# Kernel tuning notes

Hardware: AMD Instinct MI355X
Metric: run time of the kernel (lower is better)

## Reference

```python
import jax, jax.numpy as jnp
import numpy as np

HEADS = 16

def setup_inputs() -> dict:
    key = jax.random.key(0)
    k1, k2, k3 = jax.random.split(key, 3)
    B, T, C = 4, 2048, 1024
    s = 0.02
    return {
        "x": jax.random.normal(k1, (B, T, C), dtype=jnp.float32),
        "W_qkv": jax.random.normal(k2, (C, 3 * C), dtype=jnp.float32) * s,
        "b_qkv": jnp.zeros((3 * C,), dtype=jnp.float32),
        "W_pr": jax.random.normal(k3, (C, C), dtype=jnp.float32) * s,
        "b_pr": jnp.zeros((C,), dtype=jnp.float32),
    }

def reference(x, W_qkv, b_qkv, W_pr, b_pr):
    B, T, C = x.shape
    H = HEADS
    hd = C // H
    qkv = x @ W_qkv + b_qkv                     # [B,T,3C]
    q, k, v = jnp.split(qkv, 3, axis=-1)
    # [B,T,C] -> [B,H,T,hd]
    q = q.reshape(B, T, H, hd).transpose(0, 2, 1, 3)
    k = k.reshape(B, T, H, hd).transpose(0, 2, 1, 3)
    v = v.reshape(B, T, H, hd).transpose(0, 2, 1, 3)
    att = jnp.einsum('bhqd,bhkd->bhqk', q, k) * (1.0 / jnp.sqrt(jnp.float32(hd)))
    causal = jnp.tril(jnp.ones((T, T), dtype=bool))
    att = jnp.where(causal[None, None, :, :], att, jnp.float32(-jnp.inf))
    att = jax.nn.softmax(att, axis=-1)
    y = jnp.einsum('bhqk,bhkd->bhqd', att, v)   # [B,H,T,hd]
    y = y.transpose(0, 2, 1, 3).reshape(B, T, C)  # merge heads
    return y @ W_pr + b_pr
```

## Files before the change

kernel.cpp:

```cpp
#include <hip/hip_runtime.h>


typedef __attribute__((ext_vector_type(8))) short bf16x8;
typedef __attribute__((ext_vector_type(4))) float f32x4;

#define MFMA16(a, b, c) __builtin_amdgcn_mfma_f32_16x16x32_bf16(a, b, c, 0, 0, 0)

#define QK_SCALE 0.1803368801111244f

__device__ __forceinline__ unsigned short f2bf(float f) {
    union { float f; unsigned u; } v; v.f = f;
    unsigned r = v.u + 0x7fffu + ((v.u >> 16) & 1u);
    return (unsigned short)(r >> 16);
}

typedef __attribute__((address_space(1))) const unsigned int guint;
typedef __attribute__((address_space(3))) unsigned int luint;
__device__ __forceinline__ void gload16(const void* g, void* l) {
    __builtin_amdgcn_global_load_lds((guint*)g, (luint*)l, 16, 0, 0);
}

__device__ __forceinline__ float exp2_hw(float x) {
    float y;
    asm("v_exp_f32 %0, %1" : "=v"(y) : "v"(x));
    return y;
}

__device__ __forceinline__ unsigned cvt_pk_bf16(float lo, float hi) {
    unsigned w;
    asm("v_cvt_pk_bf16_f32 %0, %1, %2" : "=v"(w) : "v"(lo), "v"(hi));
    return w;
}

__global__ __launch_bounds__(256) void k_prep(
    const float* __restrict__ x, unsigned short* __restrict__ xb,
    const float* __restrict__ Wqkv, unsigned short* __restrict__ Wqt,
    const float* __restrict__ Wpr, unsigned short* __restrict__ Wpt) {
    __shared__ unsigned short tile[32][33];
    const int b = blockIdx.x;
    if (b < 8192) {
        int i = b * 256 + threadIdx.x;
        float4 v = reinterpret_cast<const float4*>(x)[i];
        ushort4 o;
        o.x = f2bf(v.x); o.y = f2bf(v.y); o.z = f2bf(v.z); o.w = f2bf(v.w);
        reinterpret_cast<ushort4*>(xb)[i] = o;
        return;
    }
    const float* W; unsigned short* Wt; int K, N, idx;
    if (b < 11264) { W = Wqkv; Wt = Wqt; K = 1024; N = 3072; idx = b - 8192;  }
    else           { W = Wpr;  Wt = Wpt; K = 1024; N = 1024; idx = b - 11264; }
    const int nb = N / 32;
    const int bn = (idx % nb) * 32, bk = (idx / nb) * 32;
    int tx = threadIdx.x & 31, ty = threadIdx.x >> 5;
#pragma unroll
    for (int i = 0; i < 32; i += 8)
        tile[ty + i][tx] = f2bf(W[(size_t)(bk + ty + i) * N + bn + tx]);
    __syncthreads();
#pragma unroll
    for (int i = 0; i < 32; i += 8)
        Wt[(size_t)(bn + ty + i) * K + bk + tx] = tile[tx][ty + i];
}


__global__ __launch_bounds__(256, 2) void k_gemm_qkv(
    const unsigned short* __restrict__ A,
    const unsigned short* __restrict__ Bt,
    const float* __restrict__ bias,
    unsigned short* __restrict__ Qo,
    unsigned short* __restrict__ Ko,
    unsigned short* __restrict__ Vto)
{
    constexpr int K = 1024;
    __shared__ alignas(16) char smem[65536];
    unsigned short* Ep = (unsigned short*)smem;
    const int tid = threadIdx.x;
    const int wave = tid >> 6, lane = tid & 63;
    const int wr = wave >> 1, wc = wave & 1;
    const int lrow = lane & 15, lkg = lane >> 4;
    const int bm = blockIdx.y * 128, bn = blockIdx.x * 128;

    const int scol = (((tid & 7) ^ ((tid >> 3) & 7)) << 3);
    const int r0 = tid >> 3;
    const unsigned short* gA[4];
    const unsigned short* gB[4];
#pragma unroll
    for (int i = 0; i < 4; ++i) {
        gA[i] = A + (size_t)(bm + i * 32 + r0) * K + scol;
        gB[i] = Bt + (size_t)(bn + i * 32 + r0) * K + scol;
    }

    f32x4 acc[4][4] = {};

#define GSTAGE(kt_, bufn_)                                          \
    do {                                                            \
        char* ba_ = smem + (bufn_) * 32768;                         \
        gload16(gA[0] + (kt_), ba_ + tid * 16);                     \
        gload16(gA[1] + (kt_), ba_ + 4096 + tid * 16);              \
        gload16(gA[2] + (kt_), ba_ + 8192 + tid * 16);              \
        gload16(gA[3] + (kt_), ba_ + 12288 + tid * 16);             \
        gload16(gB[0] + (kt_), ba_ + 16384 + tid * 16);             \
        gload16(gB[1] + (kt_), ba_ + 20480 + tid * 16);             \
        gload16(gB[2] + (kt_), ba_ + 24576 + tid * 16);             \
        gload16(gB[3] + (kt_), ba_ + 28672 + tid * 16);             \
    } while (0)

    GSTAGE(0, 0);
    int buf = 0;
    for (int t = 0; t < 16; ++t) {
        asm volatile("s_waitcnt vmcnt(0)" ::: "memory");
        __builtin_amdgcn_s_barrier();
        __builtin_amdgcn_sched_barrier(0);
        if (t < 15) GSTAGE((t + 1) * 64, buf ^ 1);

        const char* Ab = smem + buf * 32768;
        const char* Bb = Ab + 16384;
        bf16x8 af[4][2], bfr[4][2];
#pragma unroll
        for (int m = 0; m < 4; ++m) {
            int R = wr * 64 + m * 16 + lrow;
#pragma unroll
            for (int k = 0; k < 2; ++k)
                af[m][k] = *reinterpret_cast<const bf16x8*>(
                    Ab + R * 128 + (((k * 4 + lkg) ^ (R & 7)) << 4));
        }
#pragma unroll
        for (int n = 0; n < 4; ++n) {
            int R = wc * 64 + n * 16 + lrow;
#pragma unroll
            for (int k = 0; k < 2; ++k)
                bfr[n][k] = *reinterpret_cast<const bf16x8*>(
                    Bb + R * 128 + (((k * 4 + lkg) ^ (R & 7)) << 4));
        }
        __builtin_amdgcn_s_setprio(1);
#pragma unroll
        for (int m = 0; m < 4; ++m)
#pragma unroll
            for (int n = 0; n < 4; ++n) {
                acc[m][n] = MFMA16(af[m][0], bfr[n][0], acc[m][n]);
                acc[m][n] = MFMA16(af[m][1], bfr[n][1], acc[m][n]);
            }
        __builtin_amdgcn_s_setprio(0);
        buf ^= 1;
    }
#undef GSTAGE
    __syncthreads();

    const int which = bn >> 10;
    const int h0 = (bn & 1023) >> 6;
    const int bq = bm >> 11;
    const int t0 = bm & 2047;
    const float qs = (which == 0) ? QK_SCALE : 1.0f;

#pragma unroll
    for (int m = 0; m < 4; ++m) {
        int rl = wr * 64 + m * 16 + lkg * 4;
#pragma unroll
        for (int n = 0; n < 4; ++n) {
            int cl = wc * 64 + n * 16 + lrow;
            float bia = bias[bn + cl];
#pragma unroll
            for (int r = 0; r < 4; ++r) {
                unsigned short val = f2bf((acc[m][n][r] + bia) * qs);
                if (which == 2) {
                    int tl = rl + r;
                    int pt = (tl & 0x60) | ((tl & 15) << 1) | ((tl >> 4) & 1);
                    Ep[cl * 130 + pt] = val;
                } else {
                    Ep[(rl + r) * 130 + cl] = val;
                }
            }
        }
    }
    __syncthreads();

    const int chunk = tid & 15, rbase = tid >> 4;
    if (which != 2) {
        const int head = chunk >> 3, d0 = (chunk & 7) * 8;
        unsigned short* dst = (which == 0 ? Qo : Ko) +
            (size_t)((bq * 16 + h0 + head) * 2048 + t0) * 64 + d0;
#pragma unroll
        for (int s = 0; s < 8; ++s) {
            int row = s * 16 + rbase;
            bf16x8 v = *reinterpret_cast<const bf16x8*>(&Ep[row * 130 + chunk * 8]);
            *reinterpret_cast<bf16x8*>(dst + (size_t)row * 64) = v;
        }
    } else {
#pragma unroll
        for (int s = 0; s < 8; ++s) {
            int pd = s * 16 + rbase;
            bf16x8 v = *reinterpret_cast<const bf16x8*>(&Ep[pd * 130 + chunk * 8]);
            int bh = bq * 16 + h0 + (pd >> 6);
            size_t addr = ((size_t)(bh * 64 + (pd & 63)) * 2048) + t0 + chunk * 8;
            *reinterpret_cast<bf16x8*>(Vto + addr) = v;
        }
    }
}

__global__ __launch_bounds__(256, 2) void k_attn(
    const unsigned short* __restrict__ Q,
    const unsigned short* __restrict__ Kg,
    const unsigned short* __restrict__ Vt,
    unsigned short* __restrict__ Y)
{
    __shared__ alignas(16) unsigned short Ks[2][4096];
    __shared__ alignas(16) unsigned short Vs[2][4096];
    __shared__ unsigned int Pu[4][32][36];
    const int tid = threadIdx.x;
    const int wave = tid >> 6, lane = tid & 63;
    const int lrow = lane & 15, lkg = lane >> 4;
    const int bh = blockIdx.x & 63;
    const int s = (blockIdx.x >> 6) & 3;
    const int band = blockIdx.x >> 8;
    const int j = (band == 0) ? 15 - s : (band == 1) ? 8 + s : (band == 2) ? 7 - s : s;
    const int qt = 4 * j + wave;
    const int q0 = qt * 32;
    const int qmax = q0 + 31;
    const int nt = 2 * j + 2;
    const int b = bh >> 4, hh = bh & 15;

    const unsigned short* Qh = Q + (size_t)bh * 2048 * 64;
    const unsigned short* Kh = Kg + (size_t)bh * 2048 * 64;
    const unsigned short* Vh = Vt + (size_t)bh * 64 * 2048;

    const int srow = tid >> 3;
    const int swz = ((tid & 7) ^ (srow & 7)) << 3;
    const unsigned short* gK = Kh + (size_t)srow * 64 + swz;
    const unsigned short* gV = Vh + (size_t)srow * 2048 + swz;
    char* dK0 = (char*)&Ks[0][0] + tid * 16;
    char* dV0 = (char*)&Vs[0][0] + tid * 16;

    bf16x8 aq[2][2];
#pragma unroll
    for (int h = 0; h < 2; ++h)
#pragma unroll
        for (int ks = 0; ks < 2; ++ks)
            aq[h][ks] = *reinterpret_cast<const bf16x8*>(
                &Qh[(size_t)(q0 + h * 16 + lrow) * 64 + ks * 32 + lkg * 8]);

    f32x4 acc[2][4] = {};
    float lsum[2][4] = {};

#define STAGE(kb_, bufn_)                                           \
    do {                                                            \
        const unsigned short* k0_ = gK + (kb_) * 64;                \
        const unsigned short* v0_ = gV + (kb_);                     \
        char* dk_ = dK0 + (bufn_) * 8192;                           \
        char* dv_ = dV0 + (bufn_) * 8192;                           \
        gload16(k0_, dk_);                                          \
        gload16(k0_ + 2048, dk_ + 4096);                            \
        gload16(v0_, dv_);                                          \
        gload16(v0_ + 65536, dv_ + 4096);                           \
    } while (0)

    STAGE(0, 0);
    int buf = 0;

    for (int t = 0; t < nt; ++t) {
        asm volatile("s_waitcnt vmcnt(0)" ::: "memory");
        __builtin_amdgcn_s_barrier();
        __builtin_amdgcn_sched_barrier(0);
        if (t + 1 < nt) STAGE((t + 1) * 64, buf ^ 1);

        const int kb = t * 64;
        if (kb <= qmax) {
            const char* kbase = (const char*)&Ks[buf][0];
            const char* vbase = (const char*)&Vs[buf][0];

            f32x4 s_[2][4] = {};
            __builtin_amdgcn_s_setprio(1);
#pragma unroll
            for (int sub = 0; sub < 4; ++sub) {
                int krow = sub * 16 + lrow;
                bf16x8 kf0 = *reinterpret_cast<const bf16x8*>(
                    kbase + krow * 128 + ((lkg ^ (krow & 7)) << 4));
                bf16x8 kf1 = *reinterpret_cast<const bf16x8*>(
                    kbase + krow * 128 + (((4 + lkg) ^ (krow & 7)) << 4));
                s_[0][sub] = MFMA16(aq[0][0], kf0, s_[0][sub]);
                s_[0][sub] = MFMA16(aq[0][1], kf1, s_[0][sub]);
                s_[1][sub] = MFMA16(aq[1][0], kf0, s_[1][sub]);
                s_[1][sub] = MFMA16(aq[1][1], kf1, s_[1][sub]);
            }
            __builtin_amdgcn_s_setprio(0);

            const bool need_mask = (kb + 64 > q0);
#pragma unroll
            for (int h = 0; h < 2; ++h)
#pragma unroll
                for (int sub = 0; sub < 4; ++sub)
#pragma unroll
                    for (int r = 0; r < 4; ++r) {
                        float v = s_[h][sub][r];
                        if (need_mask) {
                            int key = kb + sub * 16 + lrow;
                            int q = q0 + h * 16 + lkg * 4 + r;
                            v = (key <= q) ? v : -1e30f;
                        }
                        s_[h][sub][r] = exp2_hw(v);
                    }

#pragma unroll
            for (int h = 0; h < 2; ++h) {
                int prow = h * 16 + lkg * 4;
#pragma unroll
                for (int r = 0; r < 4; ++r) {
                    lsum[h][r] += (s_[h][0][r] + s_[h][1][r]) + (s_[h][2][r] + s_[h][3][r]);
                    Pu[wave][prow + r][lrow]      = cvt_pk_bf16(s_[h][0][r], s_[h][1][r]);
                    Pu[wave][prow + r][16 + lrow] = cvt_pk_bf16(s_[h][2][r], s_[h][3][r]);
                }
            }

            bf16x8 pf[2][2];
#pragma unroll
            for (int h = 0; h < 2; ++h)
#pragma unroll
                for (int kc = 0; kc < 2; ++kc)
                    pf[h][kc] = *reinterpret_cast<const bf16x8*>(
                        &Pu[wave][h * 16 + lrow][kc * 16 + lkg * 4]);

            __builtin_amdgcn_s_setprio(1);
#pragma unroll
            for (int tt = 0; tt < 4; ++tt) {
                int vrow = tt * 16 + lrow;
                bf16x8 vf0 = *reinterpret_cast<const bf16x8*>(
                    vbase + vrow * 128 + ((lkg ^ (vrow & 7)) << 4));
                bf16x8 vf1 = *reinterpret_cast<const bf16x8*>(
                    vbase + vrow * 128 + (((4 + lkg) ^ (vrow & 7)) << 4));
                acc[0][tt] = MFMA16(pf[0][0], vf0, acc[0][tt]);
                acc[0][tt] = MFMA16(pf[0][1], vf1, acc[0][tt]);
                acc[1][tt] = MFMA16(pf[1][0], vf0, acc[1][tt]);
                acc[1][tt] = MFMA16(pf[1][1], vf1, acc[1][tt]);
            }
            __builtin_amdgcn_s_setprio(0);
        }

        buf ^= 1;
    }
#undef STAGE

#pragma unroll
    for (int h = 0; h < 2; ++h) {
        float inv[4];
#pragma unroll
        for (int r = 0; r < 4; ++r) {
            float l = lsum[h][r];
            l += __shfl_xor(l, 1); l += __shfl_xor(l, 2);
            l += __shfl_xor(l, 4); l += __shfl_xor(l, 8);
            inv[r] = 1.0f / l;
        }
#pragma unroll
        for (int t = 0; t < 4; ++t)
#pragma unroll
            for (int r = 0; r < 4; ++r) {
                int q = q0 + h * 16 + lkg * 4 + r;
                size_t idx = ((size_t)b * 2048 + q) * 1024 + hh * 64 + t * 16 + lrow;
                Y[idx] = f2bf(acc[h][t][r] * inv[r]);
            }
    }
}

__global__ __launch_bounds__(256, 2) void k_gemm_proj(
    const unsigned short* __restrict__ A,
    const unsigned short* __restrict__ Bt,
    const float* __restrict__ bias,
    float* __restrict__ out)
{
    constexpr int K = 1024;
    __shared__ alignas(16) char smem[65536];
    float* Ep2 = (float*)smem;
    const int tid = threadIdx.x;
    const int wave = tid >> 6, lane = tid & 63;
    const int wr = wave >> 1, wc = wave & 1;
    const int lrow = lane & 15, lkg = lane >> 4;
    const int bm = blockIdx.y * 128, bn = blockIdx.x * 128;

    const int scol = (((tid & 7) ^ ((tid >> 3) & 7)) << 3);
    const int r0 = tid >> 3;
    const unsigned short* gA[4];
    const unsigned short* gB[4];
#pragma unroll
    for (int i = 0; i < 4; ++i) {
        gA[i] = A + (size_t)(bm + i * 32 + r0) * K + scol;
        gB[i] = Bt + (size_t)(bn + i * 32 + r0) * K + scol;
    }

    f32x4 acc[4][4] = {};

#define GSTAGE(kt_, bufn_)                                          \
    do {                                                            \
        char* ba_ = smem + (bufn_) * 32768;                         \
        gload16(gA[0] + (kt_), ba_ + tid * 16);                     \
        gload16(gA[1] + (kt_), ba_ + 4096 + tid * 16);              \
        gload16(gA[2] + (kt_), ba_ + 8192 + tid * 16);              \
        gload16(gA[3] + (kt_), ba_ + 12288 + tid * 16);             \
        gload16(gB[0] + (kt_), ba_ + 16384 + tid * 16);             \
        gload16(gB[1] + (kt_), ba_ + 20480 + tid * 16);             \
        gload16(gB[2] + (kt_), ba_ + 24576 + tid * 16);             \
        gload16(gB[3] + (kt_), ba_ + 28672 + tid * 16);             \
    } while (0)

    GSTAGE(0, 0);
    int buf = 0;
    for (int t = 0; t < 16; ++t) {
        asm volatile("s_waitcnt vmcnt(0)" ::: "memory");
        __builtin_amdgcn_s_barrier();
        __builtin_amdgcn_sched_barrier(0);
        if (t < 15) GSTAGE((t + 1) * 64, buf ^ 1);

        const char* Ab = smem + buf * 32768;
        const char* Bb = Ab + 16384;
        bf16x8 af[4][2], bfr[4][2];
#pragma unroll
        for (int m = 0; m < 4; ++m) {
            int R = wr * 64 + m * 16 + lrow;
#pragma unroll
            for (int k = 0; k < 2; ++k)
                af[m][k] = *reinterpret_cast<const bf16x8*>(
                    Ab + R * 128 + (((k * 4 + lkg) ^ (R & 7)) << 4));
        }
#pragma unroll
        for (int n = 0; n < 4; ++n) {
            int R = wc * 64 + n * 16 + lrow;
#pragma unroll
            for (int k = 0; k < 2; ++k)
                bfr[n][k] = *reinterpret_cast<const bf16x8*>(
                    Bb + R * 128 + (((k * 4 + lkg) ^ (R & 7)) << 4));
        }
        __builtin_amdgcn_s_setprio(1);
#pragma unroll
        for (int m = 0; m < 4; ++m)
#pragma unroll
            for (int n = 0; n < 4; ++n) {
                acc[m][n] = MFMA16(af[m][0], bfr[n][0], acc[m][n]);
                acc[m][n] = MFMA16(af[m][1], bfr[n][1], acc[m][n]);
            }
        __builtin_amdgcn_s_setprio(0);
        buf ^= 1;
    }
#undef GSTAGE

    const int chunk = tid >> 3;
    const int r8 = tid & 7;
#pragma unroll
    for (int p = 0; p < 2; ++p) {
        __syncthreads();
        if (wr == p) {
#pragma unroll
            for (int m = 0; m < 4; ++m)
#pragma unroll
                for (int n = 0; n < 4; ++n) {
                    int cl = wc * 64 + n * 16 + lrow;
                    float bia = bias[bn + cl];
#pragma unroll
                    for (int r = 0; r < 4; ++r)
                        Ep2[(m * 16 + lkg * 4 + r) * 129 + cl] = acc[m][n][r] + bia;
                }
        }
        __syncthreads();
#pragma unroll
        for (int s = 0; s < 8; ++s) {
            int row = r8 * 8 + s;
            float4 v = *reinterpret_cast<const float4*>(&Ep2[row * 129 + chunk * 4]);
            *reinterpret_cast<float4*>(&out[(size_t)(bm + p * 64 + row) * 1024 + bn + chunk * 4]) = v;
        }
    }
}

extern "C" void kernel_launch(void* const* d_in, const int* in_sizes, int n_in,
                              void* d_out, int out_size, void* d_ws, size_t ws_size,
                              hipStream_t stream) {
    const float* x    = (const float*)d_in[0];
    const float* Wqkv = (const float*)d_in[1];
    const float* bqkv = (const float*)d_in[2];
    const float* Wpr  = (const float*)d_in[3];
    const float* bpr  = (const float*)d_in[4];
    float* out = (float*)d_out;

    char* ws = (char*)d_ws;
    unsigned short* xb  = (unsigned short*)(ws);
    unsigned short* Wqt = (unsigned short*)(ws + 16777216);
    unsigned short* Wpt = (unsigned short*)(ws + 23068672);
    unsigned short* Qb  = (unsigned short*)(ws + 25165824);
    unsigned short* Kb  = (unsigned short*)(ws + 41943040);
    unsigned short* Vt  = (unsigned short*)(ws + 58720256);
    unsigned short* Y   = xb;

    k_prep<<<12288, 256, 0, stream>>>(x, xb, Wqkv, Wqt, Wpr, Wpt);
    k_gemm_qkv<<<dim3(24, 64), 256, 0, stream>>>(xb, Wqt, bqkv, Qb, Kb, Vt);
    k_attn<<<1024, 256, 0, stream>>>(Qb, Kb, Vt, Y);
    k_gemm_proj<<<dim3(8, 64), 256, 0, stream>>>(Y, Wpt, bpr, out);
}
```

Before: 171.9 us.

## Widen GEMM tiles to 128x256 with 512 threads and triple-buffer LDS

Both the QKV and projection GEMMs now compute 128x256 output tiles per block with 8 waves instead of 128x128 with 4 waves. The single-stage double buffer becomes a three-slot LDS ring that prefetches two k-steps ahead, using a partial vmcnt wait. Epilogues are rewritten for the wider tile. The aim is more reuse of each A tile and better hiding of global-load latency. The cost is about 144KB of LDS per block, which allows only one block per CU, and a projection grid of only 256 blocks.

```diff
diff --git a/kernel.cpp b/kernel.cpp
--- a/kernel.cpp
+++ b/kernel.cpp
@@ -62,7 +62,7 @@
 }
 
 
-__global__ __launch_bounds__(256, 2) void k_gemm_qkv(
+__global__ __launch_bounds__(512, 2) void k_gemm_qkv(
     const unsigned short* __restrict__ A,
     const unsigned short* __restrict__ Bt,
     const float* __restrict__ bias,
@@ -71,48 +71,51 @@
     unsigned short* __restrict__ Vto)
 {
     constexpr int K = 1024;
-    __shared__ alignas(16) char smem[65536];
-    unsigned short* Ep = (unsigned short*)smem;
+    __shared__ alignas(16) char smem[147456];
     const int tid = threadIdx.x;
     const int wave = tid >> 6, lane = tid & 63;
-    const int wr = wave >> 1, wc = wave & 1;
+    const int wr = wave >> 2, wc = wave & 3;
     const int lrow = lane & 15, lkg = lane >> 4;
-    const int bm = blockIdx.y * 128, bn = blockIdx.x * 128;
+    const int bm = blockIdx.y * 128, bn = blockIdx.x * 256;
 
     const int scol = (((tid & 7) ^ ((tid >> 3) & 7)) << 3);
     const int r0 = tid >> 3;
-    const unsigned short* gA[4];
+    const unsigned short* gA[2];
     const unsigned short* gB[4];
 #pragma unroll
-    for (int i = 0; i < 4; ++i) {
-        gA[i] = A + (size_t)(bm + i * 32 + r0) * K + scol;
-        gB[i] = Bt + (size_t)(bn + i * 32 + r0) * K + scol;
-    }
+    for (int i = 0; i < 2; ++i)
+        gA[i] = A + (size_t)(bm + i * 64 + r0) * K + scol;
+#pragma unroll
+    for (int i = 0; i < 4; ++i)
+        gB[i] = Bt + (size_t)(bn + i * 64 + r0) * K + scol;
 
     f32x4 acc[4][4] = {};
 
-#define GSTAGE(kt_, bufn_)                                          \
+#define GSTAGE(kt_, slot_)                                          \
     do {                                                            \
-        char* ba_ = smem + (bufn_) * 32768;                         \
+        char* ba_ = smem + (slot_) * 49152;                         \
         gload16(gA[0] + (kt_), ba_ + tid * 16);                     \
-        gload16(gA[1] + (kt_), ba_ + 4096 + tid * 16);              \
-        gload16(gA[2] + (kt_), ba_ + 8192 + tid * 16);              \
-        gload16(gA[3] + (kt_), ba_ + 12288 + tid * 16);             \
+        gload16(gA[1] + (kt_), ba_ + 8192 + tid * 16);              \
         gload16(gB[0] + (kt_), ba_ + 16384 + tid * 16);             \
-        gload16(gB[1] + (kt_), ba_ + 20480 + tid * 16);             \
-        gload16(gB[2] + (kt_), ba_ + 24576 + tid * 16);             \
-        gload16(gB[3] + (kt_), ba_ + 28672 + tid * 16);             \
+        gload16(gB[1] + (kt_), ba_ + 24576 + tid * 16);             \
+        gload16(gB[2] + (kt_), ba_ + 32768 + tid * 16);             \
+        gload16(gB[3] + (kt_), ba_ + 40960 + tid * 16);             \
     } while (0)
 
     GSTAGE(0, 0);
-    int buf = 0;
+    GSTAGE(64, 1);
+    int cs = 0;
     for (int t = 0; t < 16; ++t) {
-        asm volatile("s_waitcnt vmcnt(0)" ::: "memory");
+        if (t < 15) asm volatile("s_waitcnt vmcnt(6)" ::: "memory");
+        else        asm volatile("s_waitcnt vmcnt(0)" ::: "memory");
         __builtin_amdgcn_s_barrier();
         __builtin_amdgcn_sched_barrier(0);
-        if (t < 15) GSTAGE((t + 1) * 64, buf ^ 1);
-
-        const char* Ab = smem + buf * 32768;
+        if (t + 2 < 16) {
+            int ns = cs + 2; if (ns >= 3) ns -= 3;
+            GSTAGE((t + 2) * 64, ns);
+        }
+
+        const char* Ab = smem + cs * 49152;
         const char* Bb = Ab + 16384;
         bf16x8 af[4][2], bfr[4][2];
 #pragma unroll
@@ -140,7 +143,7 @@
                 acc[m][n] = MFMA16(af[m][1], bfr[n][1], acc[m][n]);
             }
         __builtin_amdgcn_s_setprio(0);
-        buf ^= 1;
+        ++cs; if (cs == 3) cs = 0;
     }
 #undef GSTAGE
     __syncthreads();
@@ -150,47 +153,56 @@
     const int bq = bm >> 11;
     const int t0 = bm & 2047;
     const float qs = (which == 0) ? QK_SCALE : 1.0f;
-
-#pragma unroll
-    for (int m = 0; m < 4; ++m) {
-        int rl = wr * 64 + m * 16 + lkg * 4;
-#pragma unroll
-        for (int n = 0; n < 4; ++n) {
-            int cl = wc * 64 + n * 16 + lrow;
-            float bia = bias[bn + cl];
-#pragma unroll
-            for (int r = 0; r < 4; ++r) {
-                unsigned short val = f2bf((acc[m][n][r] + bia) * qs);
-                if (which == 2) {
-                    int tl = rl + r;
-                    int pt = (tl & 0x60) | ((tl & 15) << 1) | ((tl >> 4) & 1);
-                    Ep[cl * 130 + pt] = val;
-                } else {
-                    Ep[(rl + r) * 130 + cl] = val;
-                }
-            }
-        }
-    }
-    __syncthreads();
-
-    const int chunk = tid & 15, rbase = tid >> 4;
+    unsigned short* Ep = (unsigned short*)smem;
+
     if (which != 2) {
-        const int head = chunk >> 3, d0 = (chunk & 7) * 8;
+#pragma unroll
+        for (int m = 0; m < 4; ++m) {
+            int trow = wr * 64 + m * 16 + lkg * 4;
+#pragma unroll
+            for (int n = 0; n < 4; ++n) {
+                int cl = wc * 64 + n * 16 + lrow;
+                float bia = bias[bn + cl];
+#pragma unroll
+                for (int r = 0; r < 4; ++r)
+                    Ep[(trow + r) * 258 + cl] = f2bf((acc[m][n][r] + bia) * qs);
+            }
+        }
+        __syncthreads();
+        const int chunk = tid & 31, rbase = tid >> 5;
+        const int head = h0 + (chunk >> 3), d0 = (chunk & 7) * 8;
         unsigned short* dst = (which == 0 ? Qo : Ko) +
-            (size_t)((bq * 16 + h0 + head) * 2048 + t0) * 64 + d0;
+            (size_t)((bq * 16 + head) * 2048 + t0) * 64 + d0;
 #pragma unroll
         for (int s = 0; s < 8; ++s) {
             int row = s * 16 + rbase;
-            bf16x8 v = *reinterpret_cast<const bf16x8*>(&Ep[row * 130 + chunk * 8]);
+            bf16x8 v = *reinterpret_cast<const bf16x8*>(&Ep[row * 258 + chunk * 8]);
             *reinterpret_cast<bf16x8*>(dst + (size_t)row * 64) = v;
         }
     } else {
 #pragma unroll
+        for (int m = 0; m < 4; ++m) {
+            int tl0 = wr * 64 + m * 16 + lkg * 4;
+#pragma unroll
+            for (int n = 0; n < 4; ++n) {
+                int cl = wc * 64 + n * 16 + lrow;
+                float bia = bias[bn + cl];
+#pragma unroll
+                for (int r = 0; r < 4; ++r) {
+                    int tl = tl0 + r;
+                    int pt = (tl & 0x60) | ((tl & 15) << 1) | ((tl >> 4) & 1);
+                    Ep[cl * 130 + pt] = f2bf(acc[m][n][r] + bia);
+                }
+            }
+        }
+        __syncthreads();
+        const int chunkt = tid & 15, crow = tid >> 4;
+#pragma unroll
         for (int s = 0; s < 8; ++s) {
-            int pd = s * 16 + rbase;
-            bf16x8 v = *reinterpret_cast<const bf16x8*>(&Ep[pd * 130 + chunk * 8]);
-            int bh = bq * 16 + h0 + (pd >> 6);
-            size_t addr = ((size_t)(bh * 64 + (pd & 63)) * 2048) + t0 + chunk * 8;
+            int cl = s * 32 + crow;
+            bf16x8 v = *reinterpret_cast<const bf16x8*>(&Ep[cl * 130 + chunkt * 8]);
+            int bh = bq * 16 + h0 + (cl >> 6);
+            size_t addr = ((size_t)(bh * 64 + (cl & 63)) * 2048) + t0 + chunkt * 8;
             *reinterpret_cast<bf16x8*>(Vto + addr) = v;
         }
     }
@@ -358,55 +370,58 @@
     }
 }
 
-__global__ __launch_bounds__(256, 2) void k_gemm_proj(
+__global__ __launch_bounds__(512, 2) void k_gemm_proj(
     const unsigned short* __restrict__ A,
     const unsigned short* __restrict__ Bt,
     const float* __restrict__ bias,
     float* __restrict__ out)
 {
     constexpr int K = 1024;
-    __shared__ alignas(16) char smem[65536];
-    float* Ep2 = (float*)smem;
+    __shared__ alignas(16) char smem[147456];
     const int tid = threadIdx.x;
     const int wave = tid >> 6, lane = tid & 63;
-    const int wr = wave >> 1, wc = wave & 1;
+    const int wr = wave >> 2, wc = wave & 3;
     const int lrow = lane & 15, lkg = lane >> 4;
-    const int bm = blockIdx.y * 128, bn = blockIdx.x * 128;
+    const int bm = blockIdx.y * 128, bn = blockIdx.x * 256;
 
     const int scol = (((tid & 7) ^ ((tid >> 3) & 7)) << 3);
     const int r0 = tid >> 3;
-    const unsigned short* gA[4];
+    const unsigned short* gA[2];
     const unsigned short* gB[4];
 #pragma unroll
-    for (int i = 0; i < 4; ++i) {
-        gA[i] = A + (size_t)(bm + i * 32 + r0) * K + scol;
-        gB[i] = Bt + (size_t)(bn + i * 32 + r0) * K + scol;
-    }
+    for (int i = 0; i < 2; ++i)
+        gA[i] = A + (size_t)(bm + i * 64 + r0) * K + scol;
+#pragma unroll
+    for (int i = 0; i < 4; ++i)
+        gB[i] = Bt + (size_t)(bn + i * 64 + r0) * K + scol;
 
     f32x4 acc[4][4] = {};
 
-#define GSTAGE(kt_, bufn_)                                          \
+#define GSTAGE(kt_, slot_)                                          \
     do {                                                            \
-        char* ba_ = smem + (bufn_) * 32768;                         \
+        char* ba_ = smem + (slot_) * 49152;                         \
         gload16(gA[0] + (kt_), ba_ + tid * 16);                     \
-        gload16(gA[1] + (kt_), ba_ + 4096 + tid * 16);              \
-        gload16(gA[2] + (kt_), ba_ + 8192 + tid * 16);              \
-        gload16(gA[3] + (kt_), ba_ + 12288 + tid * 16);             \
+        gload16(gA[1] + (kt_), ba_ + 8192 + tid * 16);              \
         gload16(gB[0] + (kt_), ba_ + 16384 + tid * 16);             \
-        gload16(gB[1] + (kt_), ba_ + 20480 + tid * 16);             \
-        gload16(gB[2] + (kt_), ba_ + 24576 + tid * 16);             \
-        gload16(gB[3] + (kt_), ba_ + 28672 + tid * 16);             \
+        gload16(gB[1] + (kt_), ba_ + 24576 + tid * 16);             \
+        gload16(gB[2] + (kt_), ba_ + 32768 + tid * 16);             \
+        gload16(gB[3] + (kt_), ba_ + 40960 + tid * 16);             \
     } while (0)
 
     GSTAGE(0, 0);
-    int buf = 0;
+    GSTAGE(64, 1);
+    int cs = 0;
     for (int t = 0; t < 16; ++t) {
-        asm volatile("s_waitcnt vmcnt(0)" ::: "memory");
+        if (t < 15) asm volatile("s_waitcnt vmcnt(6)" ::: "memory");
+        else        asm volatile("s_waitcnt vmcnt(0)" ::: "memory");
         __builtin_amdgcn_s_barrier();
         __builtin_amdgcn_sched_barrier(0);
-        if (t < 15) GSTAGE((t + 1) * 64, buf ^ 1);
-
-        const char* Ab = smem + buf * 32768;
+        if (t + 2 < 16) {
+            int ns = cs + 2; if (ns >= 3) ns -= 3;
+            GSTAGE((t + 2) * 64, ns);
+        }
+
+        const char* Ab = smem + cs * 49152;
         const char* Bb = Ab + 16384;
         bf16x8 af[4][2], bfr[4][2];
 #pragma unroll
@@ -434,34 +449,32 @@
                 acc[m][n] = MFMA16(af[m][1], bfr[n][1], acc[m][n]);
             }
         __builtin_amdgcn_s_setprio(0);
-        buf ^= 1;
+        ++cs; if (cs == 3) cs = 0;
     }
 #undef GSTAGE
-
-    const int chunk = tid >> 3;
-    const int r8 = tid & 7;
-#pragma unroll
-    for (int p = 0; p < 2; ++p) {
-        __syncthreads();
-        if (wr == p) {
-#pragma unroll
-            for (int m = 0; m < 4; ++m)
-#pragma unroll
-                for (int n = 0; n < 4; ++n) {
-                    int cl = wc * 64 + n * 16 + lrow;
-                    float bia = bias[bn + cl];
-#pragma unroll
-                    for (int r = 0; r < 4; ++r)
-                        Ep2[(m * 16 + lkg * 4 + r) * 129 + cl] = acc[m][n][r] + bia;
-                }
-        }
-        __syncthreads();
-#pragma unroll
-        for (int s = 0; s < 8; ++s) {
-            int row = r8 * 8 + s;
-            float4 v = *reinterpret_cast<const float4*>(&Ep2[row * 129 + chunk * 4]);
-            *reinterpret_cast<float4*>(&out[(size_t)(bm + p * 64 + row) * 1024 + bn + chunk * 4]) = v;
-        }
+    __syncthreads();
+
+    float* Ep2 = (float*)smem;
+#pragma unroll
+    for (int m = 0; m < 4; ++m) {
+        int row0 = wr * 64 + m * 16 + lkg * 4;
+#pragma unroll
+        for (int n = 0; n < 4; ++n) {
+            int cl = wc * 64 + n * 16 + lrow;
+            float bia = bias[bn + cl];
+#pragma unroll
+            for (int r = 0; r < 4; ++r)
+                Ep2[(row0 + r) * 257 + cl] = acc[m][n][r] + bia;
+        }
+    }
+    __syncthreads();
+    const int chunk = tid & 63, rbase = tid >> 6;
+#pragma unroll
+    for (int s = 0; s < 16; ++s) {
+        int row = s * 8 + rbase;
+        float4 v = *reinterpret_cast<const float4*>(&Ep2[row * 257 + chunk * 4]);
+        *reinterpret_cast<float4*>(
+            &out[(size_t)(bm + row) * 1024 + bn + chunk * 4]) = v;
     }
 }
 
@@ -485,7 +498,7 @@
     unsigned short* Y   = xb;
 
     k_prep<<<12288, 256, 0, stream>>>(x, xb, Wqkv, Wqt, Wpr, Wpt);
-    k_gemm_qkv<<<dim3(24, 64), 256, 0, stream>>>(xb, Wqt, bqkv, Qb, Kb, Vt);
+    k_gemm_qkv<<<dim3(12, 64), 512, 0, stream>>>(xb, Wqt, bqkv, Qb, Kb, Vt);
     k_attn<<<1024, 256, 0, stream>>>(Qb, Kb, Vt, Y);
-    k_gemm_proj<<<dim3(8, 64), 256, 0, stream>>>(Y, Wpt, bpr, out);
-}
+    k_gemm_proj<<<dim3(4, 64), 512, 0, stream>>>(Y, Wpt, bpr, out);
+}
```

After: 167.7 us. 2.4% less time.
